# Performance work log

Hardware: AMD Instinct MI355X
Metric: run time of the kernel (lower is better)

The kernel has to match this reference:

```python
import jax, jax.numpy as jnp
import numpy as np

BBOX_POS_MAX = 1024.0
BN_EPS = 1e-5


def _bn_eval(x, g, b, rm, rv):
    # BatchNorm1d in eval mode: affine transform with running stats
    return g * (x - rm) * jax.lax.rsqrt(rv + BN_EPS) + b


def setup_inputs() -> dict:
    key = jax.random.key(0)
    ks = jax.random.split(key, 24)
    B, N, F = 32, 512, 1024
    E = 32768
    H1, H2, H3 = 512, 256, 128          # node_pred_hidden
    EH1, EH2 = 64, 64                   # edge_pred_hidden
    NC, EC = 8, 10                      # node/edge concept channels
    BC = 9                              # bbox_channels (4 bbox + 4 dir + 1 prio)
    s = 0.02
    inp = {
        'roi_features': jax.random.normal(ks[0], (B, N, F), jnp.float32),
        'batch_bboxes': jax.random.uniform(ks[1], (B, N, 4), jnp.float32) * BBOX_POS_MAX,
        'batch_directions': jax.random.uniform(ks[2], (B, N, 4), jnp.float32),
        'batch_priorities': jax.random.uniform(ks[3], (B, N), jnp.float32),
        'batch_edge_index': jax.random.randint(ks[4], (B, 2, E), 0, N, jnp.int32),
        # node_predictor params
        'np_w1': jax.random.normal(ks[5], (F, H1), jnp.float32) * s,
        'np_b1': jnp.zeros((H1,), jnp.float32),
        'bn1_g': jnp.ones((H1,), jnp.float32),
        'bn1_b': jnp.zeros((H1,), jnp.float32),
        'bn1_rm': jnp.zeros((H1,), jnp.float32),
        'bn1_rv': jnp.ones((H1,), jnp.float32),
        'np_w2': jax.random.normal(ks[6], (H1, H2), jnp.float32) * s,
        'np_b2': jnp.zeros((H2,), jnp.float32),
        'bn2_g': jnp.ones((H2,), jnp.float32),
        'bn2_b': jnp.zeros((H2,), jnp.float32),
        'bn2_rm': jnp.zeros((H2,), jnp.float32),
        'bn2_rv': jnp.ones((H2,), jnp.float32),
        'np_w3': jax.random.normal(ks[7], (H2, H3), jnp.float32) * s,
        'np_b3': jnp.zeros((H3,), jnp.float32),
        'ni_w': jax.random.normal(ks[8], (H3, NC), jnp.float32) * s,
        'ni_b': jnp.zeros((NC,), jnp.float32),
        # edge_predictor params (input dim = 2 * bbox_channels)
        'ep_w1': jax.random.normal(ks[9], (2 * BC, EH1), jnp.float32) * s,
        'ep_b1': jnp.zeros((EH1,), jnp.float32),
        'ep_w2': jax.random.normal(ks[10], (EH1, EH2), jnp.float32) * s,
        'ep_b2': jnp.zeros((EH2,), jnp.float32),
        'ei_w': jax.random.normal(ks[11], (EH2, EC), jnp.float32) * s,
        'ei_b': jnp.zeros((EC,), jnp.float32),
    }
    return inp


def reference(roi_features, batch_bboxes, batch_directions, batch_priorities,
              batch_edge_index,
              np_w1, np_b1, bn1_g, bn1_b, bn1_rm, bn1_rv,
              np_w2, np_b2, bn2_g, bn2_b, bn2_rm, bn2_rv,
              np_w3, np_b3, ni_w, ni_b,
              ep_w1, ep_b1, ep_w2, ep_b2, ei_w, ei_b):
    B, N, F = roi_features.shape
    # ---- node path: MLP (eval-mode BN, dropout = identity) + sigmoid interpreter
    x = roi_features.reshape(B * N, F)
    h = jax.nn.relu(_bn_eval(x @ np_w1 + np_b1, bn1_g, bn1_b, bn1_rm, bn1_rv))
    h = jax.nn.relu(_bn_eval(h @ np_w2 + np_b2, bn2_g, bn2_b, bn2_rm, bn2_rv))
    h = jax.nn.relu(h @ np_w3 + np_b3)
    node_concepts = jax.nn.sigmoid(h @ ni_w + ni_b).reshape(B, N, -1)
    # ---- edge path: per-batch gather of node attrs via edge_index, concat, MLP
    node_attr = jnp.concatenate(
        [batch_bboxes / BBOX_POS_MAX, batch_directions, batch_priorities[..., None]],
        axis=-1)  # [B, N, 9]
    C = node_attr.shape[-1]
    src_idx = batch_edge_index[:, 0, :, None]  # [B, E, 1]
    dst_idx = batch_edge_index[:, 1, :, None]
    src = jnp.take_along_axis(node_attr, src_idx.astype(jnp.int32), axis=1)  # [B, E, 9]
    dst = jnp.take_along_axis(node_attr, dst_idx.astype(jnp.int32), axis=1)
    edge_attr = jnp.concatenate([src, dst], axis=-1).reshape(-1, 2 * C)  # [B*E, 18]
    e = jax.nn.relu(edge_attr @ ep_w1 + ep_b1)
    e = jax.nn.relu(e @ ep_w2 + ep_b2)
    edge_concepts = jax.nn.sigmoid(e @ ei_w + ei_b)  # [B*E, EC]
    return node_concepts, edge_concepts
```

## Files before the change

### kernel.cpp

```cpp
#include <hip/hip_runtime.h>
#include <cstdint>
#include <cstddef>

#define BN_EPSF 1e-5f

constexpr int B_  = 32, N_ = 512, F_ = 1024, E_ = 32768;
constexpr int H1_ = 512, H2_ = 256, H3_ = 128, NC_ = 8, EC_ = 10;
constexpr int M_  = B_ * N_;
constexpr int NE_ = B_ * E_;

typedef short bf16x8 __attribute__((ext_vector_type(8)));
typedef float f32x4  __attribute__((ext_vector_type(4)));

__device__ __forceinline__ short f2bf(float f) {
  union { float f; unsigned u; } v; v.f = f;
  unsigned r = v.u + 0x7fffu + ((v.u >> 16) & 1u);
  return (short)(r >> 16);
}
__device__ __forceinline__ unsigned cvtpk(float a, float b) {
  unsigned r;
  asm("v_cvt_pk_bf16_f32 %0, %1, %2" : "=v"(r) : "v"(a), "v"(b));
  return r;
}

#define GLDS(gp, lp) __builtin_amdgcn_global_load_lds( \
    (const __attribute__((address_space(1))) void*)(gp), \
    (__attribute__((address_space(3))) void*)(lp), 16, 0, 0)

#define MFMA(a, b, c) __builtin_amdgcn_mfma_f32_16x16x32_bf16((a), (b), (c), 0, 0, 0)

__device__ __forceinline__ void wt_body(
    const float* __restrict__ W, short* __restrict__ Wt, int K, int N,
    int bx, int by, float (*s)[33])
{
  const int tx = threadIdx.x & 31, ty = threadIdx.x >> 5;
  const int k0 = by * 32, n0 = bx * 32;
#pragma unroll
  for (int r = 0; r < 4; r++)
    s[ty * 4 + r][tx] = W[(size_t)(k0 + ty * 4 + r) * N + n0 + tx];
  __syncthreads();
#pragma unroll
  for (int r = 0; r < 4; r++)
    Wt[(size_t)(n0 + ty * 4 + r) * K + k0 + tx] = f2bf(s[tx][ty * 4 + r]);
}

__global__ __launch_bounds__(256) void k_prep(
    const float* __restrict__ roi, ushort* __restrict__ roiB,
    const float* __restrict__ w1, short* __restrict__ w1t,
    const float* __restrict__ w2, short* __restrict__ w2t,
    const float* __restrict__ w3, short* __restrict__ w3t,
    const float* __restrict__ bbox, const float* __restrict__ dir,
    const float* __restrict__ pri, ushort* __restrict__ attrT)
{
  __shared__ float s[32][33];
  const int bx = blockIdx.x;
  if (bx < 8192) {
    int i = bx * 256 + threadIdx.x;
    float4 a = *(const float4*)(roi + (size_t)i * 8);
    float4 b = *(const float4*)(roi + (size_t)i * 8 + 4);
    unsigned o[4];
    o[0] = cvtpk(a.x, a.y); o[1] = cvtpk(a.z, a.w);
    o[2] = cvtpk(b.x, b.y); o[3] = cvtpk(b.z, b.w);
    *(uint4*)(roiB + (size_t)i * 8) = *(uint4*)o;
  } else if (bx < 8704) {
    int idx = bx - 8192; wt_body(w1, w1t, F_, H1_, idx & 15, idx >> 4, s);
  } else if (bx < 8832) {
    int idx = bx - 8704; wt_body(w2, w2t, H1_, H2_, idx & 7, idx >> 3, s);
  } else if (bx < 8864) {
    int idx = bx - 8832; wt_body(w3, w3t, H2_, H3_, idx & 3, idx >> 2, s);
  } else {
    int gi = (bx - 8864) * 256 + threadIdx.x;
    const float inv = 1.0f / 1024.0f;
    float4 bv = *(const float4*)(bbox + (size_t)gi * 4);
    float4 dv = *(const float4*)(dir + (size_t)gi * 4);
    float pp = pri[gi];
    uint4 lo, hi;
    lo.x = cvtpk(bv.x * inv, bv.y * inv); lo.y = cvtpk(bv.z * inv, bv.w * inv);
    lo.z = cvtpk(dv.x, dv.y);             lo.w = cvtpk(dv.z, dv.w);
    hi.x = cvtpk(pp, 0.f); hi.y = 0; hi.z = 0; hi.w = 0;
    *(uint4*)(attrT + (size_t)gi * 16)     = lo;
    *(uint4*)(attrT + (size_t)gi * 16 + 8) = hi;
  }
}

__device__ __forceinline__ void relu_pack_shuf(
    const f32x4 (&acc)[4], int la, int lb, bool lo32, bf16x8 (&out)[2])
{
  unsigned plo[4], phi[4];
#pragma unroll
  for (int t = 0; t < 4; t++) {
    plo[t] = cvtpk(fmaxf(acc[t][0], 0.f), fmaxf(acc[t][1], 0.f));
    phi[t] = cvtpk(fmaxf(acc[t][2], 0.f), fmaxf(acc[t][3], 0.f));
  }
#pragma unroll
  for (int ks = 0; ks < 2; ks++) {
    unsigned w0a = (unsigned)__shfl((int)plo[2 * ks], la);
    unsigned w0b = (unsigned)__shfl((int)plo[2 * ks + 1], la);
    unsigned w1a = (unsigned)__shfl((int)phi[2 * ks], la);
    unsigned w1b = (unsigned)__shfl((int)phi[2 * ks + 1], la);
    unsigned w2a = (unsigned)__shfl((int)plo[2 * ks], lb);
    unsigned w2b = (unsigned)__shfl((int)plo[2 * ks + 1], lb);
    unsigned w3a = (unsigned)__shfl((int)phi[2 * ks], lb);
    unsigned w3b = (unsigned)__shfl((int)phi[2 * ks + 1], lb);
    union { unsigned u[4]; bf16x8 v; } t;
    t.u[0] = lo32 ? w0a : w0b;
    t.u[1] = lo32 ? w1a : w1b;
    t.u[2] = lo32 ? w2a : w2b;
    t.u[3] = lo32 ? w3a : w3b;
    out[ks] = t.v;
  }
}

__global__ __launch_bounds__(256, 3) void k_fused(
    const ushort* __restrict__ attrT, const int* __restrict__ eidx,
    const float* __restrict__ ew1, const float* __restrict__ eb1,
    const float* __restrict__ ew2, const float* __restrict__ eb2,
    const float* __restrict__ eow, const float* __restrict__ eob,
    float* __restrict__ out_edge,
    const short* __restrict__ roiB, const short* __restrict__ w1t,
    const float* __restrict__ b1, const float* __restrict__ g1,
    const float* __restrict__ bb1, const float* __restrict__ rm1,
    const float* __restrict__ rv1, short* __restrict__ h1)
{
  __shared__ __align__(16) char arena[32768];

  const int bx = blockIdx.x;
  const int rsel = bx % 3;
  const int tid  = threadIdx.x;
  const int wave = tid >> 6, lane = tid & 63;
  const int lm = lane & 15;

  if (rsel == 2) {
    const int lb = bx / 3;
    short* As = (short*)arena;
    short* Bs = (short*)(arena + 16384);
    const int m0 = (lb >> 2) * 128, n0 = (lb & 3) * 128;
    const int wm = wave >> 1, wn = wave & 1;
    const int q  = lane >> 4;
    const int srow = tid >> 3;
    const int sko  = ((tid & 7) ^ (srow & 7)) * 8;

    f32x4 acc[4][4] = {};
    for (int k0 = 0; k0 < F_; k0 += 64) {
#pragma unroll
      for (int it = 0; it < 4; it++)
        GLDS(roiB + (size_t)(m0 + it * 32 + srow) * F_ + k0 + sko,
             (char*)As + it * 4096 + wave * 1024);
#pragma unroll
      for (int it = 0; it < 4; it++)
        GLDS(w1t + (size_t)(n0 + it * 32 + srow) * F_ + k0 + sko,
             (char*)Bs + it * 4096 + wave * 1024);
      __syncthreads();

#pragma unroll
      for (int ks = 0; ks < 2; ks++) {
        const int co = (((ks * 4 + q) ^ (lm & 7)) * 8);
        bf16x8 af[4], bfr[4];
#pragma unroll
        for (int t = 0; t < 4; t++) {
          af[t]  = *(const bf16x8*)&As[(wm * 64 + t * 16 + lm) * 64 + co];
          bfr[t] = *(const bf16x8*)&Bs[(wn * 64 + t * 16 + lm) * 64 + co];
        }
#pragma unroll
        for (int ti = 0; ti < 4; ti++)
#pragma unroll
          for (int tj = 0; tj < 4; tj++)
            acc[ti][tj] = MFMA(af[ti], bfr[tj], acc[ti][tj]);
      }
      __syncthreads();
    }
#pragma unroll
    for (int tj = 0; tj < 4; tj++) {
      const int col = n0 + wn * 64 + tj * 16 + lm;
      const float bi = b1[col];
      float s = g1[col] * rsqrtf(rv1[col] + BN_EPSF);
      float t = bb1[col] - rm1[col] * s;
#pragma unroll
      for (int ti = 0; ti < 4; ti++) {
        const int rbase = m0 + wm * 64 + ti * 16 + ((lane >> 4) << 2);
#pragma unroll
        for (int r = 0; r < 4; r += 2) {
          float va = fmaf(acc[ti][tj][r]     + bi, s, t);
          float vb = fmaf(acc[ti][tj][r + 1] + bi, s, t);
          unsigned p = cvtpk(fmaxf(va, 0.f), fmaxf(vb, 0.f));
          h1[(size_t)(rbase + r)     * H1_ + col] = (short)p;
          h1[(size_t)(rbase + r + 1) * H1_ + col] = (short)(p >> 16);
        }
      }
    }
    return;
  }

  const int eb    = (bx / 3) * 2 + rsel;
  const int batch = eb >> 5;
  const int q     = lane >> 4;

  short*  sW1 = (short*)arena;
  short*  sW2 = (short*)(arena + 4096);
  short*  sW3 = (short*)(arena + 12288);
  ushort* sA0 = (ushort*)(arena + 14336);
  ushort* sA1 = (ushort*)(arena + 22528);

  for (int i = tid; i < 2048; i += 256) {
    int n = i >> 5, k = i & 31;
    short v = 0;
    if (k < 9)                  v = f2bf(ew1[k * 64 + n]);
    else if (k >= 16 && k < 25) v = f2bf(ew1[(k - 7) * 64 + n]);
    sW1[i] = v;
  }
  for (int i = tid; i < 4096; i += 256) {
    int n = i >> 6, k = i & 63;
    sW2[i] = f2bf(ew2[k * 64 + n]);
  }
  for (int i = tid; i < 1024; i += 256) {
    int n = i >> 6, k = i & 63;
    sW3[i] = (n < 10) ? f2bf(eow[k * 10 + n]) : (short)0;
  }
  {
    const ushort* atg = attrT + (size_t)batch * 512 * 16;
    for (int n = tid; n < 512; n += 256) {
      uint4 lo = *(const uint4*)(atg + n * 16);
      uint4 hi = *(const uint4*)(atg + n * 16 + 8);
      *(uint4*)&sA0[n * 8] = lo;
      *(uint4*)&sA1[n * 8] = hi;
    }
  }
  __syncthreads();

  bf16x8 fW1[4], fW2[4][2], fW3[2];
#pragma unroll
  for (int t = 0; t < 4; t++)
    fW1[t] = *(const bf16x8*)&sW1[(t * 16 + lm) * 32 + q * 8];
#pragma unroll
  for (int t = 0; t < 4; t++)
#pragma unroll
    for (int ks = 0; ks < 2; ks++)
      fW2[t][ks] = *(const bf16x8*)&sW2[(t * 16 + lm) * 64 + ks * 32 + q * 8];
#pragma unroll
  for (int ks = 0; ks < 2; ks++)
    fW3[ks] = *(const bf16x8*)&sW3[lm * 64 + ks * 32 + q * 8];

  f32x4 b1q[4], b2q[4], boq;
#pragma unroll
  for (int t = 0; t < 4; t++) {
    b1q[t] = *(const f32x4*)(eb1 + t * 16 + q * 4);
    b2q[t] = *(const f32x4*)(eb2 + t * 16 + q * 4);
  }
#pragma unroll
  for (int r = 0; r < 4; r++)
    boq[r] = (q * 4 + r < 10) ? eob[q * 4 + r] : 0.f;

  const int  la   = (lane & 15) | ((lane & 16) << 1);
  const int  lbn  = la + 16;
  const bool lo32 = (lane < 32);
  const int* ip   = eidx + (size_t)batch * 2 * E_ + ((lane >= 32) ? E_ : 0);
  const int  ebl  = (eb & 31) * 1024;
  const ushort* sAsel = (lane & 16) ? sA1 : sA0;

  int nidx[8][2];
#pragma unroll
  for (int b = 0; b < 8; b++)
#pragma unroll
    for (int ti = 0; ti < 2; ti++)
      nidx[b][ti] = ip[ebl + b * 128 + wave * 32 + ti * 16 + lm];

  bf16x8 xf[2];
#pragma unroll
  for (int ti = 0; ti < 2; ti++)
    xf[ti] = *(const bf16x8*)&sAsel[nidx[0][ti] * 8];

#pragma unroll
  for (int bi = 0; bi < 8; bi++) {
    bf16x8 xn[2];
    if (bi < 7) {
#pragma unroll
      for (int ti = 0; ti < 2; ti++)
        xn[ti] = *(const bf16x8*)&sAsel[nidx[bi + 1][ti] * 8];
    }

    f32x4 acc1[2][4];
#pragma unroll
    for (int tj = 0; tj < 4; tj++)
#pragma unroll
      for (int ti = 0; ti < 2; ti++)
        acc1[ti][tj] = MFMA(fW1[tj], xf[ti], b1q[tj]);
    bf16x8 xf2[2][2];
#pragma unroll
    for (int ti = 0; ti < 2; ti++)
      relu_pack_shuf(acc1[ti], la, lbn, lo32, xf2[ti]);

    f32x4 acc2[2][4];
#pragma unroll
    for (int ti = 0; ti < 2; ti++)
#pragma unroll
      for (int tj = 0; tj < 4; tj++)
        acc2[ti][tj] = b2q[tj];
#pragma unroll
    for (int ks = 0; ks < 2; ks++)
#pragma unroll
      for (int tj = 0; tj < 4; tj++)
#pragma unroll
        for (int ti = 0; ti < 2; ti++)
          acc2[ti][tj] = MFMA(fW2[tj][ks], xf2[ti][ks], acc2[ti][tj]);
    bf16x8 xf3[2][2];
#pragma unroll
    for (int ti = 0; ti < 2; ti++)
      relu_pack_shuf(acc2[ti], la, lbn, lo32, xf3[ti]);

#pragma unroll
    for (int ti = 0; ti < 2; ti++) {
      f32x4 a3 = boq;
#pragma unroll
      for (int ks = 0; ks < 2; ks++)
        a3 = MFMA(fW3[ks], xf3[ti][ks], a3);
      float o[4];
#pragma unroll
      for (int r = 0; r < 4; r++)
        o[r] = 1.f / (1.f + __expf(-a3[r]));
      size_t base = (size_t)(eb * 1024 + bi * 128 + wave * 32 + ti * 16 + lm) * 10;
      if (q == 0) {
        float2 t0; t0.x = o[0]; t0.y = o[1]; *(float2*)(out_edge + base)     = t0;
        float2 t1; t1.x = o[2]; t1.y = o[3]; *(float2*)(out_edge + base + 2) = t1;
      } else if (q == 1) {
        float2 t0; t0.x = o[0]; t0.y = o[1]; *(float2*)(out_edge + base + 4) = t0;
        float2 t1; t1.x = o[2]; t1.y = o[3]; *(float2*)(out_edge + base + 6) = t1;
      } else if (q == 2) {
        float2 t0; t0.x = o[0]; t0.y = o[1]; *(float2*)(out_edge + base + 8) = t0;
      }
    }
    xf[0] = xn[0]; xf[1] = xn[1];
  }
}

#define STAGE_A(bufA, bufB, k0) do {                                        \
    { int c_ = tid >> 7, row_ = (tid >> 2) & 31;                            \
      GLDS(h1 + (size_t)(m0 + row_) * 512 + (k0) + c_ * 32 + skq,           \
           (char*)(bufA) + wave * 1024); }                                  \
    _Pragma("unroll")                                                       \
    for (int it = 0; it < 4; it++)                                          \
      _Pragma("unroll")                                                     \
      for (int c = 0; c < 2; c++)                                           \
        GLDS(w2t + (size_t)(it * 64 + srow) * 512 + (k0) + c * 32 + skq,    \
             (char*)(bufB) + c * 16384 + it * 4096 + wave * 1024);          \
  } while (0)

#define COMP_A(bufA, bufB) do {                                             \
    _Pragma("unroll")                                                       \
    for (int c = 0; c < 2; c++) {                                           \
      bf16x8 af = *(const bf16x8*)&((const short*)(bufA))                   \
          [c * 1024 + (wm * 16 + lm) * 32 + sq];                            \
      _Pragma("unroll")                                                     \
      for (int nt = 0; nt < 8; nt++) {                                      \
        bf16x8 bfr = *(const bf16x8*)&((const short*)(bufB))                \
            [c * 8192 + (wn * 128 + nt * 16 + lm) * 32 + sq];               \
        acc2[nt] = MFMA(af, bfr, acc2[nt]);                                 \
      } } } while (0)

#define STAGE_B(bufB, k0) do {                                              \
    _Pragma("unroll")                                                       \
    for (int it = 0; it < 2; it++)                                          \
      _Pragma("unroll")                                                     \
      for (int c = 0; c < 2; c++)                                           \
        GLDS(w3t + (size_t)(it * 64 + srow) * 256 + (k0) + c * 32 + skq,    \
             (char*)(bufB) + c * 8192 + it * 4096 + wave * 1024);           \
  } while (0)

#define COMP_B(bufB, k0) do {                                               \
    _Pragma("unroll")                                                       \
    for (int c = 0; c < 2; c++) {                                           \
      bf16x8 af = *(const bf16x8*)&sH2[(wm * 16 + lm) * 264                 \
          + (k0) + c * 32 + q * 8];                                         \
      _Pragma("unroll")                                                     \
      for (int nt = 0; nt < 4; nt++) {                                      \
        bf16x8 bfr = *(const bf16x8*)&((const short*)(bufB))                \
            [c * 4096 + (wn * 64 + nt * 16 + lm) * 32 + sq];                \
        acc3[nt] = MFMA(af, bfr, acc3[nt]);                                 \
      } } } while (0)

__global__ __launch_bounds__(256) void k_tail(
    const short* __restrict__ h1, const short* __restrict__ w2t,
    const short* __restrict__ w3t,
    const float* __restrict__ b2, const float* __restrict__ g2,
    const float* __restrict__ bb2, const float* __restrict__ rm2,
    const float* __restrict__ rv2,
    const float* __restrict__ b3, const float* __restrict__ niw,
    const float* __restrict__ nib, float* __restrict__ out)
{
  __shared__ __align__(16) char arena[73728];
  char* const A0 = arena;          char* const A1 = arena + 4096;
  char* const Bb0 = arena + 8192;  char* const Bb1 = arena + 40960;
  char* const B3a = arena + 20480; char* const B3b = arena + 36864;
  short* sH2 = (short*)arena;
  short* sH3 = (short*)(arena + 53248);

  const int tid  = threadIdx.x;
  const int wave = tid >> 6, lane = tid & 63;
  const int lm = lane & 15, q = lane >> 4;
  const int wm = wave >> 1, wn = wave & 1;
  const int m0 = blockIdx.x * 32;
  const int srow = tid >> 2;
  const int skq  = ((tid & 3) ^ ((tid >> 3) & 3)) * 8;
  const int sq   = (q ^ ((lm >> 1) & 3)) * 8;

  f32x4 acc2[8] = {};
  STAGE_A(A0, Bb0, 0);
  __syncthreads();
#pragma unroll
  for (int t = 0; t < 8; t += 2) {
    if (t + 1 < 8) STAGE_A(A1, Bb1, (t + 1) * 64);
    COMP_A(A0, Bb0);
    __syncthreads();
    if (t + 2 < 8) STAGE_A(A0, Bb0, (t + 2) * 64);
    COMP_A(A1, Bb1);
    __syncthreads();
  }
#pragma unroll
  for (int nt = 0; nt < 8; nt++) {
    int col = wn * 128 + nt * 16 + lm;
    float s = g2[col] * rsqrtf(rv2[col] + BN_EPSF);
    float t = bb2[col] - rm2[col] * s;
    float bi = b2[col];
    float v0 = fmaf(acc2[nt][0] + bi, s, t);
    float v1 = fmaf(acc2[nt][1] + bi, s, t);
    float v2 = fmaf(acc2[nt][2] + bi, s, t);
    float v3 = fmaf(acc2[nt][3] + bi, s, t);
    unsigned p01 = cvtpk(fmaxf(v0, 0.f), fmaxf(v1, 0.f));
    unsigned p23 = cvtpk(fmaxf(v2, 0.f), fmaxf(v3, 0.f));
    int rb = wm * 16 + q * 4;
    sH2[(rb + 0) * 264 + col] = (short)p01;
    sH2[(rb + 1) * 264 + col] = (short)(p01 >> 16);
    sH2[(rb + 2) * 264 + col] = (short)p23;
    sH2[(rb + 3) * 264 + col] = (short)(p23 >> 16);
  }
  STAGE_B(B3a, 0);
  __syncthreads();

  f32x4 acc3[4] = {};
#pragma unroll
  for (int t = 0; t < 4; t += 2) {
    if (t + 1 < 4) STAGE_B(B3b, (t + 1) * 64);
    COMP_B(B3a, t * 64);
    __syncthreads();
    if (t + 2 < 4) STAGE_B(B3a, (t + 2) * 64);
    COMP_B(B3b, (t + 1) * 64);
    __syncthreads();
  }
#pragma unroll
  for (int nt = 0; nt < 4; nt++) {
    int col = wn * 64 + nt * 16 + lm;
    float bi = b3[col];
    float v0 = acc3[nt][0] + bi;
    float v1 = acc3[nt][1] + bi;
    float v2 = acc3[nt][2] + bi;
    float v3 = acc3[nt][3] + bi;
    unsigned p01 = cvtpk(fmaxf(v0, 0.f), fmaxf(v1, 0.f));
    unsigned p23 = cvtpk(fmaxf(v2, 0.f), fmaxf(v3, 0.f));
    int rb = wm * 16 + q * 4;
    sH3[(rb + 0) * 136 + col] = (short)p01;
    sH3[(rb + 1) * 136 + col] = (short)(p01 >> 16);
    sH3[(rb + 2) * 136 + col] = (short)p23;
    sH3[(rb + 3) * 136 + col] = (short)(p23 >> 16);
  }
  __syncthreads();

  if (wave < 2) {
    f32x4 a4 = {};
#pragma unroll
    for (int c = 0; c < 4; c++) {
      ushort tmp[8];
#pragma unroll
      for (int j = 0; j < 8; j++) {
        int k = c * 32 + q * 8 + j;
        tmp[j] = (lm < 8) ? (ushort)f2bf(niw[k * 8 + lm]) : (ushort)0;
      }
      bf16x8 fw = *(bf16x8*)tmp;
      bf16x8 af4 = *(const bf16x8*)&sH3[(wave * 16 + lm) * 136 + c * 32 + q * 8];
      a4 = MFMA(af4, fw, a4);
    }
    if (lm < 8) {
      float bi = nib[lm];
#pragma unroll
      for (int r = 0; r < 4; r++) {
        float v = a4[r] + bi;
        out[(size_t)(m0 + wave * 16 + q * 4 + r) * 8 + lm] = 1.f / (1.f + __expf(-v));
      }
    }
  }
}

extern "C" void kernel_launch(void* const* d_in, const int* in_sizes, int n_in,
                              void* d_out, int out_size, void* d_ws, size_t ws_size,
                              hipStream_t stream)
{
  const float* roi   = (const float*)d_in[0];
  const float* bbox  = (const float*)d_in[1];
  const float* dir   = (const float*)d_in[2];
  const float* pri   = (const float*)d_in[3];
  const int*   eidx  = (const int*)d_in[4];
  const float* w1    = (const float*)d_in[5];
  const float* b1    = (const float*)d_in[6];
  const float* g1    = (const float*)d_in[7];
  const float* bb1   = (const float*)d_in[8];
  const float* rm1   = (const float*)d_in[9];
  const float* rv1   = (const float*)d_in[10];
  const float* w2    = (const float*)d_in[11];
  const float* b2    = (const float*)d_in[12];
  const float* g2    = (const float*)d_in[13];
  const float* bb2   = (const float*)d_in[14];
  const float* rm2   = (const float*)d_in[15];
  const float* rv2   = (const float*)d_in[16];
  const float* w3    = (const float*)d_in[17];
  const float* b3    = (const float*)d_in[18];
  const float* niw   = (const float*)d_in[19];
  const float* nib   = (const float*)d_in[20];
  const float* ew1   = (const float*)d_in[21];
  const float* eb1   = (const float*)d_in[22];
  const float* ew2   = (const float*)d_in[23];
  const float* eb2   = (const float*)d_in[24];
  const float* eow   = (const float*)d_in[25];
  const float* eob   = (const float*)d_in[26];

  float* out_node = (float*)d_out;
  float* out_edge = (float*)d_out + (size_t)M_ * NC_;

  char* w = (char*)d_ws;
  short*  roiB  = (short*)w;
  short*  w1t   = (short*)(w + 33554432);
  short*  w2t   = (short*)(w + 34603008);
  short*  w3t   = (short*)(w + 34865152);
  ushort* attrT = (ushort*)(w + 34930688);
  short*  h1    = (short*)(w + 35717120);

  k_prep<<<8928, 256, 0, stream>>>(roi, (ushort*)roiB, w1, w1t, w2, w2t,
                                   w3, w3t, bbox, dir, pri, attrT);

  k_fused<<<1536, 256, 0, stream>>>(
      attrT, eidx, ew1, eb1, ew2, eb2, eow, eob, out_edge,
      roiB, w1t, b1, g1, bb1, rm1, rv1, h1);

  k_tail<<<M_ / 32, 256, 0, stream>>>(
      h1, w2t, w3t, b2, g2, bb2, rm2, rv2, b3, niw, nib, out_node);
}
```

Before: 235.5 us.

## Double-buffer layer-1 GEMM LDS tiles with K=32 stages to overlap loads

```diff
diff --git a/kernel.cpp b/kernel.cpp
--- a/kernel.cpp
+++ b/kernel.cpp
@@ -132,41 +132,53 @@
 
   if (rsel == 2) {
     const int lb = bx / 3;
-    short* As = (short*)arena;
-    short* Bs = (short*)(arena + 16384);
+    char* const As0 = arena;
+    char* const As1 = arena + 8192;
+    char* const Bs0 = arena + 16384;
+    char* const Bs1 = arena + 24576;
     const int m0 = (lb >> 2) * 128, n0 = (lb & 3) * 128;
     const int wm = wave >> 1, wn = wave & 1;
     const int q  = lane >> 4;
-    const int srow = tid >> 3;
-    const int sko  = ((tid & 7) ^ (srow & 7)) * 8;
+    const int arow = tid >> 2;
+    const int sko  = ((tid & 3) ^ (arow & 3)) * 8;
+    const int co   = (q ^ (lm & 3)) * 8;
+
+#define L1S(Ab, Bb, k0) do {                                              \
+      _Pragma("unroll")                                                   \
+      for (int it = 0; it < 2; it++)                                      \
+        GLDS(roiB + (size_t)(m0 + it * 64 + arow) * F_ + (k0) + sko,      \
+             (char*)(Ab) + it * 4096 + wave * 1024);                      \
+      _Pragma("unroll")                                                   \
+      for (int it = 0; it < 2; it++)                                      \
+        GLDS(w1t + (size_t)(n0 + it * 64 + arow) * F_ + (k0) + sko,       \
+             (char*)(Bb) + it * 4096 + wave * 1024);                      \
+    } while (0)
+
+#define L1C(Ab, Bb) do {                                                  \
+      bf16x8 af[4], bfr[4];                                               \
+      _Pragma("unroll")                                                   \
+      for (int t = 0; t < 4; t++) {                                       \
+        af[t]  = *(const bf16x8*)&((const short*)(Ab))                    \
+                     [(wm * 64 + t * 16 + lm) * 32 + co];                 \
+        bfr[t] = *(const bf16x8*)&((const short*)(Bb))                    \
+                     [(wn * 64 + t * 16 + lm) * 32 + co];                 \
+      }                                                                   \
+      _Pragma("unroll")                                                   \
+      for (int ti = 0; ti < 4; ti++)                                      \
+        _Pragma("unroll")                                                 \
+        for (int tj = 0; tj < 4; tj++)                                    \
+          acc[ti][tj] = MFMA(af[ti], bfr[tj], acc[ti][tj]);               \
+    } while (0)
 
     f32x4 acc[4][4] = {};
+    L1S(As0, Bs0, 0);
+    __syncthreads();
     for (int k0 = 0; k0 < F_; k0 += 64) {
-#pragma unroll
-      for (int it = 0; it < 4; it++)
-        GLDS(roiB + (size_t)(m0 + it * 32 + srow) * F_ + k0 + sko,
-             (char*)As + it * 4096 + wave * 1024);
-#pragma unroll
-      for (int it = 0; it < 4; it++)
-        GLDS(w1t + (size_t)(n0 + it * 32 + srow) * F_ + k0 + sko,
-             (char*)Bs + it * 4096 + wave * 1024);
+      if (k0 + 32 < F_) L1S(As1, Bs1, k0 + 32);
+      L1C(As0, Bs0);
       __syncthreads();
-
-#pragma unroll
-      for (int ks = 0; ks < 2; ks++) {
-        const int co = (((ks * 4 + q) ^ (lm & 7)) * 8);
-        bf16x8 af[4], bfr[4];
-#pragma unroll
-        for (int t = 0; t < 4; t++) {
-          af[t]  = *(const bf16x8*)&As[(wm * 64 + t * 16 + lm) * 64 + co];
-          bfr[t] = *(const bf16x8*)&Bs[(wn * 64 + t * 16 + lm) * 64 + co];
-        }
-#pragma unroll
-        for (int ti = 0; ti < 4; ti++)
-#pragma unroll
-          for (int tj = 0; tj < 4; tj++)
-            acc[ti][tj] = MFMA(af[ti], bfr[tj], acc[ti][tj]);
-      }
+      if (k0 + 64 < F_) L1S(As0, Bs0, k0 + 64);
+      L1C(As1, Bs1);
       __syncthreads();
     }
 #pragma unroll
```

After: 239.0 us. No clear change (+1.5%).
